# Optimization experiments

Hardware: AMD Instinct MI355X
Metric: run time of the kernel (lower is better)

Reference implementation:

```python
import jax, jax.numpy as jnp
import numpy as np

IN_DIM = 512
OUT_DIM = 512
DEGREE = 3
KNOTS = (0.2, 0.4, 0.6, 0.8)
SDIM = DEGREE + 1 + len(KNOTS)  # 8
BATCH = 2048


def truncated_power_basis(t):
    # t: (B,) -> (B, SDIM)
    cols = [jnp.ones_like(t)]
    for p in range(1, DEGREE + 1):
        cols.append(t ** p)
    for c in KNOTS:  # degree > 1 branch: relu(t - knot)^degree
        cols.append(jax.nn.relu(t - c) ** DEGREE)
    return jnp.stack(cols, axis=1)


def setup_inputs() -> dict:
    key = jax.random.key(0)
    k0, k1, k2 = jax.random.split(key, 3)
    inputs = jax.random.uniform(k0, (BATCH, IN_DIM + 1), dtype=jnp.float32)
    # xavier_uniform for W_wts (fan_in=SDIM, fan_out=IN_DIM*OUT_DIM)
    limW = float(np.sqrt(6.0 / (SDIM + IN_DIM * OUT_DIM)))
    W_wts = jax.random.uniform(k1, (SDIM, IN_DIM * OUT_DIM), dtype=jnp.float32,
                               minval=-limW, maxval=limW)
    limb = float(np.sqrt(6.0 / (SDIM + OUT_DIM)))
    b_wts = jax.random.uniform(k2, (SDIM, OUT_DIM), dtype=jnp.float32,
                               minval=-limb, maxval=limb)
    return {"inputs": inputs, "W_wts": W_wts, "b_wts": b_wts}


def reference(inputs, W_wts, b_wts):
    treatment = inputs[:, 0]          # (B,)
    features = inputs[:, 1:]          # (B, IN_DIM)
    basis = truncated_power_basis(treatment)  # (B, SDIM)
    Wk = W_wts.reshape(SDIM, IN_DIM, OUT_DIM)
    # fused: per-sample weight W[b] = sum_s basis[b,s] * Wk[s]; out[b] = features[b] @ W[b]
    out = jnp.einsum('bs,bi,sio->bo', basis, features, Wk)
    out = out + basis @ b_wts         # (B, OUT_DIM)
    return out
```

## Files before the change

kernel.cpp:

```cpp
#include <hip/hip_runtime.h>
#include <stdint.h>

#define BATCH   2048
#define INDIM   512
#define OUTDIM  512
#define KTOT    4096
#define NBLK_A  2048
#define NBLK_B  512
#define SPLITK  4
#define KSTEPS  16

typedef __attribute__((ext_vector_type(4))) float  f32x4;
typedef __attribute__((ext_vector_type(8))) __bf16 bf16x8;
typedef __attribute__((ext_vector_type(8))) unsigned short u16x8;
typedef __attribute__((ext_vector_type(4))) unsigned short u16x4;

__device__ __forceinline__ unsigned short f2bf(float x) {
  unsigned int u = __float_as_uint(x);
  u += 0x7fffu + ((u >> 16) & 1u);
  return (unsigned short)(u >> 16);
}

__device__ __forceinline__ void llds16(const void* g, void* s) {
  __builtin_amdgcn_global_load_lds(
      (__attribute__((address_space(1))) void*)g,
      (__attribute__((address_space(3))) void*)s, 16, 0, 0);
}

__global__ __launch_bounds__(256) void prep_kernel(
    const float* __restrict__ inp, const float* __restrict__ W,
    const float* __restrict__ bwts, unsigned short* __restrict__ Abf,
    unsigned short* __restrict__ Btf, float* __restrict__ out) {
  const int tid = threadIdx.x;
  const int bx  = blockIdx.x;
  if (bx < NBLK_A) {
    const float* row = inp + (size_t)bx * (INDIM + 1);
    const float t = row[0];
    float bs[8];
    bs[0] = 1.0f; bs[1] = t; bs[2] = t * t; bs[3] = bs[2] * t;
    const float kn[4] = {0.2f, 0.4f, 0.6f, 0.8f};
#pragma unroll
    for (int c = 0; c < 4; ++c) {
      float d = fmaxf(t - kn[c], 0.0f);
      bs[4 + c] = d * d * d;
    }
    unsigned short* Arow = Abf + (size_t)bx * KTOT;
#pragma unroll
    for (int it = 0; it < 4; ++it) {
      const int k4 = tid * 4 + it * 1024;
      const float s = bs[k4 >> 9];
      const int i = k4 & 511;
      u16x4 o;
      o.x = f2bf(s * row[1 + i]); o.y = f2bf(s * row[2 + i]);
      o.z = f2bf(s * row[3 + i]); o.w = f2bf(s * row[4 + i]);
      *(u16x4*)&Arow[k4] = o;
    }
    float* orow = out + (size_t)bx * OUTDIM;
#pragma unroll
    for (int rep = 0; rep < 2; ++rep) {
      const int o = tid + rep * 256;
      float acc = 0.f;
#pragma unroll
      for (int s = 0; s < 8; ++s) acc += bs[s] * bwts[s * OUTDIM + o];
      orow[o] = acc;
    }
  } else {
    const int bb = bx - NBLK_A;
    const int kt = bb >> 3, ntile = bb & 7;
    const int k0 = kt * 64, n0 = ntile * 64;
    __shared__ float Ts[64][65];
#pragma unroll
    for (int p = 0; p < 4; ++p) {
      const int r  = (tid >> 4) + p * 16;
      const int c4 = (tid & 15) * 4;
      float4 v = *(const float4*)&W[(size_t)(k0 + r) * 512 + n0 + c4];
      Ts[c4 + 0][r] = v.x; Ts[c4 + 1][r] = v.y;
      Ts[c4 + 2][r] = v.z; Ts[c4 + 3][r] = v.w;
    }
    __syncthreads();
    const int nl  = tid >> 2;
    const int kcc = (tid & 3) * 16;
    u16x8 o0, o1;
#pragma unroll
    for (int q = 0; q < 8; ++q) {
      o0[q] = f2bf(Ts[nl][kcc + q]);
      o1[q] = f2bf(Ts[nl][kcc + 8 + q]);
    }
    unsigned short* dst = Btf + (size_t)(n0 + nl) * KTOT + k0 + kcc;
    *(u16x8*)dst = o0;
    *(u16x8*)(dst + 8) = o1;
  }
}

__global__ __launch_bounds__(256, 4) void gemm_kernel(
    const unsigned short* __restrict__ Abf,
    const unsigned short* __restrict__ Btf,
    float* __restrict__ out) {
  const int tid  = threadIdx.x;
  const int xcd  = blockIdx.x & 7;
  const int slot = blockIdx.x >> 3;
  const int kc    = xcd & 3;
  const int mhalf = xcd >> 2;
  const int nt    = slot & 7;
  const int mt    = mhalf * 16 + (slot >> 3);
  const int m0 = mt * 64, n0 = nt * 64;
  const int l = tid & 63, w = tid >> 6;
  const int wm = w >> 1, wn = w & 1;
  const int quad = l >> 4, lr = l & 15;

  __shared__ __align__(16) unsigned short As[64 * 64];
  __shared__ __align__(16) unsigned short Bs[64 * 64];

  f32x4 acc00 = {}, acc01 = {}, acc10 = {}, acc11 = {};

  const int sr = tid >> 3, pc = tid & 7;
  const int lc = pc ^ (sr & 7);
  const unsigned short* Ag = Abf + (size_t)(m0 + sr) * KTOT + lc * 8;
  const unsigned short* Bg = Btf + (size_t)(n0 + sr) * KTOT + lc * 8;
  unsigned short* AsW = &As[sr * 64 + pc * 8];
  unsigned short* BsW = &Bs[sr * 64 + pc * 8];

  const int sx  = lr & 7;
  const int ar  = (wm * 32 + lr) * 64;
  const int br  = (wn * 32 + lr) * 64;
  const int c0  = ((0 + quad) ^ sx) * 8;
  const int c1  = ((4 + quad) ^ sx) * 8;

  int koff = kc * (KSTEPS * 64);
  for (int it = 0; it < KSTEPS; ++it) {
    llds16(Ag + koff,            AsW);
    llds16(Ag + koff + 32 * KTOT, AsW + 32 * 64);
    llds16(Bg + koff,            BsW);
    llds16(Bg + koff + 32 * KTOT, BsW + 32 * 64);
    __syncthreads();

    bf16x8 a00 = *(const bf16x8*)&As[ar + c0];
    bf16x8 a10 = *(const bf16x8*)&As[ar + 1024 + c0];
    bf16x8 b00 = *(const bf16x8*)&Bs[br + c0];
    bf16x8 b10 = *(const bf16x8*)&Bs[br + 1024 + c0];
    bf16x8 a01 = *(const bf16x8*)&As[ar + c1];
    bf16x8 a11 = *(const bf16x8*)&As[ar + 1024 + c1];
    bf16x8 b01 = *(const bf16x8*)&Bs[br + c1];
    bf16x8 b11 = *(const bf16x8*)&Bs[br + 1024 + c1];

    acc00 = __builtin_amdgcn_mfma_f32_16x16x32_bf16(a00, b00, acc00, 0, 0, 0);
    acc01 = __builtin_amdgcn_mfma_f32_16x16x32_bf16(a00, b10, acc01, 0, 0, 0);
    acc10 = __builtin_amdgcn_mfma_f32_16x16x32_bf16(a10, b00, acc10, 0, 0, 0);
    acc11 = __builtin_amdgcn_mfma_f32_16x16x32_bf16(a10, b10, acc11, 0, 0, 0);
    acc00 = __builtin_amdgcn_mfma_f32_16x16x32_bf16(a01, b01, acc00, 0, 0, 0);
    acc01 = __builtin_amdgcn_mfma_f32_16x16x32_bf16(a01, b11, acc01, 0, 0, 0);
    acc10 = __builtin_amdgcn_mfma_f32_16x16x32_bf16(a11, b01, acc10, 0, 0, 0);
    acc11 = __builtin_amdgcn_mfma_f32_16x16x32_bf16(a11, b11, acc11, 0, 0, 0);

    __syncthreads();
    koff += 64;
  }

  const int col = n0 + wn * 32 + lr;
  const int row = m0 + wm * 32 + quad * 4;
  float* o00 = out + (size_t)row * OUTDIM + col;
#pragma unroll
  for (int r = 0; r < 4; ++r) {
    unsafeAtomicAdd(o00 + (size_t)r * OUTDIM,             acc00[r]);
    unsafeAtomicAdd(o00 + (size_t)r * OUTDIM + 16,        acc01[r]);
    unsafeAtomicAdd(o00 + (size_t)(16 + r) * OUTDIM,      acc10[r]);
    unsafeAtomicAdd(o00 + (size_t)(16 + r) * OUTDIM + 16, acc11[r]);
  }
}

extern "C" void kernel_launch(void* const* d_in, const int* in_sizes, int n_in,
                              void* d_out, int out_size, void* d_ws, size_t ws_size,
                              hipStream_t stream) {
  const float* inp  = (const float*)d_in[0];
  const float* W    = (const float*)d_in[1];
  const float* bwts = (const float*)d_in[2];
  float* out = (float*)d_out;

  unsigned short* Abf = (unsigned short*)d_ws;
  unsigned short* Btf = Abf + (size_t)BATCH * KTOT;

  prep_kernel<<<NBLK_A + NBLK_B, 256, 0, stream>>>(inp, W, bwts, Abf, Btf, out);
  gemm_kernel<<<(BATCH / 64) * (OUTDIM / 64) * SPLITK, 256, 0, stream>>>(Abf, Btf, out);
}
```

Before: 100.7 us.

## Factor basis scaling out of A and run per-basis GEMMs with 128x128 tiles

The expanded A matrix (features scaled by each basis term, 2048x4096 bf16) is no longer materialized. Only the bf16 features and the per-row basis values are stored. Each GEMM block now takes one basis index s and computes features @ W_s on a 128x128 tile with a 4x4 MFMA fragment layout, then scales rows by basis[s] before the atomic add. This cuts A-side prep writes and reads eightfold and raises reuse per tile. The cost is fewer, heavier blocks at lower occupancy, with 8-way atomic contention per output element.

```diff
diff --git a/kernel.cpp b/kernel.cpp
--- a/kernel.cpp
+++ b/kernel.cpp
@@ -4,16 +4,11 @@
 #define BATCH   2048
 #define INDIM   512
 #define OUTDIM  512
-#define KTOT    4096
-#define NBLK_A  2048
-#define NBLK_B  512
-#define SPLITK  4
-#define KSTEPS  16
+#define SDIM    8
 
 typedef __attribute__((ext_vector_type(4))) float  f32x4;
 typedef __attribute__((ext_vector_type(8))) __bf16 bf16x8;
 typedef __attribute__((ext_vector_type(8))) unsigned short u16x8;
-typedef __attribute__((ext_vector_type(4))) unsigned short u16x4;
 
 __device__ __forceinline__ unsigned short f2bf(float x) {
   unsigned int u = __float_as_uint(x);
@@ -29,12 +24,15 @@
 
 __global__ __launch_bounds__(256) void prep_kernel(
     const float* __restrict__ inp, const float* __restrict__ W,
-    const float* __restrict__ bwts, unsigned short* __restrict__ Abf,
-    unsigned short* __restrict__ Btf, float* __restrict__ out) {
+    const float* __restrict__ bwts, unsigned short* __restrict__ Fbf,
+    unsigned short* __restrict__ Btf, float* __restrict__ basisArr,
+    float* __restrict__ out) {
   const int tid = threadIdx.x;
   const int bx  = blockIdx.x;
-  if (bx < NBLK_A) {
-    const float* row = inp + (size_t)bx * (INDIM + 1);
+  if (bx < 512) {
+    const int r = bx * 4 + (tid >> 6);
+    const int l = tid & 63;
+    const float* row = inp + (size_t)r * (INDIM + 1);
     const float t = row[0];
     float bs[8];
     bs[0] = 1.0f; bs[1] = t; bs[2] = t * t; bs[3] = bs[2] * t;
@@ -44,36 +42,32 @@
       float d = fmaxf(t - kn[c], 0.0f);
       bs[4 + c] = d * d * d;
     }
-    unsigned short* Arow = Abf + (size_t)bx * KTOT;
+    const int c = l * 8;
+    u16x8 o;
 #pragma unroll
-    for (int it = 0; it < 4; ++it) {
-      const int k4 = tid * 4 + it * 1024;
-      const float s = bs[k4 >> 9];
-      const int i = k4 & 511;
-      u16x4 o;
-      o.x = f2bf(s * row[1 + i]); o.y = f2bf(s * row[2 + i]);
-      o.z = f2bf(s * row[3 + i]); o.w = f2bf(s * row[4 + i]);
-      *(u16x4*)&Arow[k4] = o;
+    for (int q = 0; q < 8; ++q) o[q] = f2bf(row[1 + c + q]);
+    *(u16x8*)&Fbf[(size_t)r * INDIM + c] = o;
+    if (l < 8) basisArr[r * 8 + l] = bs[l];
+    f32x4 a0 = {}, a1 = {};
+#pragma unroll
+    for (int s = 0; s < 8; ++s) {
+      f32x4 w0 = *(const f32x4*)&bwts[s * OUTDIM + c];
+      f32x4 w1 = *(const f32x4*)&bwts[s * OUTDIM + c + 4];
+      a0 += w0 * bs[s]; a1 += w1 * bs[s];
     }
-    float* orow = out + (size_t)bx * OUTDIM;
-#pragma unroll
-    for (int rep = 0; rep < 2; ++rep) {
-      const int o = tid + rep * 256;
-      float acc = 0.f;
-#pragma unroll
-      for (int s = 0; s < 8; ++s) acc += bs[s] * bwts[s * OUTDIM + o];
-      orow[o] = acc;
-    }
+    *(f32x4*)&out[(size_t)r * OUTDIM + c]     = a0;
+    *(f32x4*)&out[(size_t)r * OUTDIM + c + 4] = a1;
   } else {
-    const int bb = bx - NBLK_A;
-    const int kt = bb >> 3, ntile = bb & 7;
-    const int k0 = kt * 64, n0 = ntile * 64;
+    const int bb = bx - 512;
+    const int kt = bb >> 3, nt = bb & 7;
+    const int ks0 = kt * 64, n0 = nt * 64;
+    const int s = ks0 >> 9, kloc0 = ks0 & 511;
     __shared__ float Ts[64][65];
 #pragma unroll
     for (int p = 0; p < 4; ++p) {
       const int r  = (tid >> 4) + p * 16;
       const int c4 = (tid & 15) * 4;
-      float4 v = *(const float4*)&W[(size_t)(k0 + r) * 512 + n0 + c4];
+      float4 v = *(const float4*)&W[(size_t)(ks0 + r) * 512 + n0 + c4];
       Ts[c4 + 0][r] = v.x; Ts[c4 + 1][r] = v.y;
       Ts[c4 + 2][r] = v.z; Ts[c4 + 3][r] = v.w;
     }
@@ -86,85 +80,82 @@
       o0[q] = f2bf(Ts[nl][kcc + q]);
       o1[q] = f2bf(Ts[nl][kcc + 8 + q]);
     }
-    unsigned short* dst = Btf + (size_t)(n0 + nl) * KTOT + k0 + kcc;
+    unsigned short* dst = Btf + (size_t)s * (512 * 512)
+                        + (size_t)(n0 + nl) * 512 + kloc0 + kcc;
     *(u16x8*)dst = o0;
     *(u16x8*)(dst + 8) = o1;
   }
 }
 
-__global__ __launch_bounds__(256, 4) void gemm_kernel(
-    const unsigned short* __restrict__ Abf,
+__global__ __launch_bounds__(256, 2) void gemm_kernel(
+    const unsigned short* __restrict__ Fbf,
     const unsigned short* __restrict__ Btf,
+    const float* __restrict__ basisArr,
     float* __restrict__ out) {
   const int tid  = threadIdx.x;
-  const int xcd  = blockIdx.x & 7;
+  const int s    = blockIdx.x & 7;
   const int slot = blockIdx.x >> 3;
-  const int kc    = xcd & 3;
-  const int mhalf = xcd >> 2;
-  const int nt    = slot & 7;
-  const int mt    = mhalf * 16 + (slot >> 3);
-  const int m0 = mt * 64, n0 = nt * 64;
+  const int nt = slot & 3, mt = slot >> 2;
+  const int m0 = mt * 128, n0 = nt * 128;
   const int l = tid & 63, w = tid >> 6;
   const int wm = w >> 1, wn = w & 1;
-  const int quad = l >> 4, lr = l & 15;
+  const int quad = l >> 4, lr = l & 15, sx = lr & 7;
 
-  __shared__ __align__(16) unsigned short As[64 * 64];
-  __shared__ __align__(16) unsigned short Bs[64 * 64];
+  __shared__ __align__(16) unsigned short As[128 * 64];
+  __shared__ __align__(16) unsigned short Bs[128 * 64];
 
-  f32x4 acc00 = {}, acc01 = {}, acc10 = {}, acc11 = {};
+  f32x4 acc[4][4] = {};
 
   const int sr = tid >> 3, pc = tid & 7;
   const int lc = pc ^ (sr & 7);
-  const unsigned short* Ag = Abf + (size_t)(m0 + sr) * KTOT + lc * 8;
-  const unsigned short* Bg = Btf + (size_t)(n0 + sr) * KTOT + lc * 8;
+  const unsigned short* Fg = Fbf + (size_t)(m0 + sr) * 512 + lc * 8;
+  const unsigned short* Bg = Btf + (size_t)s * (512 * 512)
+                           + (size_t)(n0 + sr) * 512 + lc * 8;
   unsigned short* AsW = &As[sr * 64 + pc * 8];
   unsigned short* BsW = &Bs[sr * 64 + pc * 8];
 
-  const int sx  = lr & 7;
-  const int ar  = (wm * 32 + lr) * 64;
-  const int br  = (wn * 32 + lr) * 64;
-  const int c0  = ((0 + quad) ^ sx) * 8;
-  const int c1  = ((4 + quad) ^ sx) * 8;
-
-  int koff = kc * (KSTEPS * 64);
-  for (int it = 0; it < KSTEPS; ++it) {
-    llds16(Ag + koff,            AsW);
-    llds16(Ag + koff + 32 * KTOT, AsW + 32 * 64);
-    llds16(Bg + koff,            BsW);
-    llds16(Bg + koff + 32 * KTOT, BsW + 32 * 64);
+  for (int it = 0; it < 8; ++it) {
+    const int i0 = it * 64;
+#pragma unroll
+    for (int p = 0; p < 4; ++p) {
+      llds16(Fg + i0 + p * 32 * 512, AsW + p * 2048);
+      llds16(Bg + i0 + p * 32 * 512, BsW + p * 2048);
+    }
     __syncthreads();
-
-    bf16x8 a00 = *(const bf16x8*)&As[ar + c0];
-    bf16x8 a10 = *(const bf16x8*)&As[ar + 1024 + c0];
-    bf16x8 b00 = *(const bf16x8*)&Bs[br + c0];
-    bf16x8 b10 = *(const bf16x8*)&Bs[br + 1024 + c0];
-    bf16x8 a01 = *(const bf16x8*)&As[ar + c1];
-    bf16x8 a11 = *(const bf16x8*)&As[ar + 1024 + c1];
-    bf16x8 b01 = *(const bf16x8*)&Bs[br + c1];
-    bf16x8 b11 = *(const bf16x8*)&Bs[br + 1024 + c1];
-
-    acc00 = __builtin_amdgcn_mfma_f32_16x16x32_bf16(a00, b00, acc00, 0, 0, 0);
-    acc01 = __builtin_amdgcn_mfma_f32_16x16x32_bf16(a00, b10, acc01, 0, 0, 0);
-    acc10 = __builtin_amdgcn_mfma_f32_16x16x32_bf16(a10, b00, acc10, 0, 0, 0);
-    acc11 = __builtin_amdgcn_mfma_f32_16x16x32_bf16(a10, b10, acc11, 0, 0, 0);
-    acc00 = __builtin_amdgcn_mfma_f32_16x16x32_bf16(a01, b01, acc00, 0, 0, 0);
-    acc01 = __builtin_amdgcn_mfma_f32_16x16x32_bf16(a01, b11, acc01, 0, 0, 0);
-    acc10 = __builtin_amdgcn_mfma_f32_16x16x32_bf16(a11, b01, acc10, 0, 0, 0);
-    acc11 = __builtin_amdgcn_mfma_f32_16x16x32_bf16(a11, b11, acc11, 0, 0, 0);
-
+#pragma unroll
+    for (int ks = 0; ks < 2; ++ks) {
+      const int ch = ((ks * 4 + quad) ^ sx) * 8;
+      bf16x8 af[4], bfr[4];
+#pragma unroll
+      for (int mf = 0; mf < 4; ++mf)
+        af[mf] = *(const bf16x8*)&As[(wm * 64 + mf * 16 + lr) * 64 + ch];
+#pragma unroll
+      for (int nf = 0; nf < 4; ++nf)
+        bfr[nf] = *(const bf16x8*)&Bs[(wn * 64 + nf * 16 + lr) * 64 + ch];
+#pragma unroll
+      for (int mf = 0; mf < 4; ++mf)
+#pragma unroll
+        for (int nf = 0; nf < 4; ++nf)
+          acc[mf][nf] = __builtin_amdgcn_mfma_f32_16x16x32_bf16(
+              af[mf], bfr[nf], acc[mf][nf], 0, 0, 0);
+    }
     __syncthreads();
-    koff += 64;
   }
 
-  const int col = n0 + wn * 32 + lr;
-  const int row = m0 + wm * 32 + quad * 4;
-  float* o00 = out + (size_t)row * OUTDIM + col;
 #pragma unroll
-  for (int r = 0; r < 4; ++r) {
-    unsafeAtomicAdd(o00 + (size_t)r * OUTDIM,             acc00[r]);
-    unsafeAtomicAdd(o00 + (size_t)r * OUTDIM + 16,        acc01[r]);
-    unsafeAtomicAdd(o00 + (size_t)(16 + r) * OUTDIM,      acc10[r]);
-    unsafeAtomicAdd(o00 + (size_t)(16 + r) * OUTDIM + 16, acc11[r]);
+  for (int mf = 0; mf < 4; ++mf) {
+    const int rb = m0 + wm * 64 + mf * 16 + quad * 4;
+    float bsv[4];
+#pragma unroll
+    for (int r = 0; r < 4; ++r) bsv[r] = basisArr[(rb + r) * 8 + s];
+#pragma unroll
+    for (int nf = 0; nf < 4; ++nf) {
+      const int col = n0 + wn * 64 + nf * 16 + lr;
+#pragma unroll
+      for (int r = 0; r < 4; ++r)
+        unsafeAtomicAdd(out + (size_t)(rb + r) * OUTDIM + col,
+                        bsv[r] * acc[mf][nf][r]);
+    }
   }
 }
 
@@ -176,9 +167,10 @@
   const float* bwts = (const float*)d_in[2];
   float* out = (float*)d_out;
 
-  unsigned short* Abf = (unsigned short*)d_ws;
-  unsigned short* Btf = Abf + (size_t)BATCH * KTOT;
+  unsigned short* Fbf = (unsigned short*)d_ws;
+  unsigned short* Btf = Fbf + (size_t)BATCH * INDIM;
+  float* basisArr = (float*)(Btf + (size_t)SDIM * 512 * 512);
 
-  prep_kernel<<<NBLK_A + NBLK_B, 256, 0, stream>>>(inp, W, bwts, Abf, Btf, out);
-  gemm_kernel<<<(BATCH / 64) * (OUTDIM / 64) * SPLITK, 256, 0, stream>>>(Abf, Btf, out);
+  prep_kernel<<<1024, 256, 0, stream>>>(inp, W, bwts, Fbf, Btf, basisArr, out);
+  gemm_kernel<<<512, 256, 0, stream>>>(Fbf, Btf, basisArr, out);
 }
```

Result: no change. 101.8 us (+1.1%).
